# Performance work log

Hardware: AMD Instinct MI355X
Metric: run time of the kernel (lower is better)

The kernel has to match this reference:

```python
import jax, jax.numpy as jnp
import numpy as np

NUM_HEADS = 12


def setup_inputs() -> dict:
    key = jax.random.key(0)
    ks = jax.random.split(key, 6)
    dim = 384
    B, N = 2048, 49
    nW = 64
    return {
        "x": jax.random.normal(ks[0], (B, N, dim), dtype=jnp.float32),
        "mask": jax.random.normal(ks[1], (nW, N, N), dtype=jnp.float32),
        "qkv_w": jax.random.normal(ks[2], (3 * dim, dim), dtype=jnp.float32) * 0.02,
        "qkv_b": jax.random.normal(ks[3], (3 * dim,), dtype=jnp.float32) * 0.02,
        "proj_w": jax.random.normal(ks[4], (dim, dim), dtype=jnp.float32) * 0.02,
        "proj_b": jax.random.normal(ks[5], (dim,), dtype=jnp.float32) * 0.02,
    }


def reference(x, mask, qkv_w, qkv_b, proj_w, proj_b):
    B, N, C = x.shape
    H = NUM_HEADS
    Dh = C // H
    scale = Dh ** -0.5
    nW = mask.shape[0]

    # qkv projection: [B, N, 3C]
    qkv = x @ qkv_w.T + qkv_b
    q, k, v = jnp.split(qkv, 3, axis=-1)

    def heads(t):  # [B, N, C] -> [B, H, N, Dh]
        return t.reshape(B, N, H, Dh).transpose(0, 2, 1, 3)

    q, k, v = heads(q) * scale, heads(k), heads(v)

    # [B, H, N, N] attention scores
    attn = jnp.einsum("bhnd,bhmd->bhnm", q, k)
    # add per-window additive mask: reshape B -> (B//nW, nW)
    attn = attn.reshape(B // nW, nW, H, N, N) + mask[None, :, None, :, :]
    attn = jax.nn.softmax(attn.reshape(B, H, N, N), axis=-1)

    out = jnp.einsum("bhnm,bhmd->bhnd", attn, v)
    out = out.transpose(0, 2, 1, 3).reshape(B, N, C)
    return out @ proj_w.T + proj_b
```

## Files before the change

### kernel.cpp

```cpp
#include <hip/hip_runtime.h>
#include <hip/hip_bf16.h>
#include <stdint.h>

typedef unsigned short u16;
typedef __attribute__((ext_vector_type(8))) short short8;
typedef __attribute__((ext_vector_type(4))) float f32x4;

__device__ inline u16 f2bf(float f) {
    union { float f; unsigned int u; } x; x.f = f;
    unsigned int u = x.u;
    unsigned int r = (u + 0x7FFFu + ((u >> 16) & 1u)) >> 16;
    return (u16)r;
}

__device__ inline void gld_lds16(const u16* g, u16* l) {
    auto const* gp = reinterpret_cast<const __attribute__((address_space(1))) unsigned int*>(
        reinterpret_cast<uintptr_t>(g));
    auto* lp = reinterpret_cast<__attribute__((address_space(3))) unsigned int*>(
        reinterpret_cast<uintptr_t>(l));
    __builtin_amdgcn_global_load_lds(gp, lp, 16, 0, 0);
}

#define NX8 4816896
#define NQ8 55296
#define NP8 18432
__global__ __launch_bounds__(256) void prep_all(const float* __restrict__ x,
                                                const float* __restrict__ qw,
                                                const float* __restrict__ pw,
                                                u16* __restrict__ xb,
                                                u16* __restrict__ wq,
                                                u16* __restrict__ wp) {
    size_t i = (size_t)blockIdx.x * 256 + threadIdx.x;
    const float* src; u16* dst; size_t off;
    if (i < NX8)            { src = x;  dst = xb; off = i; }
    else if (i < NX8 + NQ8) { src = qw; dst = wq; off = i - NX8; }
    else                    { src = pw; dst = wp; off = i - (NX8 + NQ8); }
    float4 v0 = ((const float4*)src)[off * 2];
    float4 v1 = ((const float4*)src)[off * 2 + 1];
    u16 h[8];
    h[0] = f2bf(v0.x); h[1] = f2bf(v0.y); h[2] = f2bf(v0.z); h[3] = f2bf(v0.w);
    h[4] = f2bf(v1.x); h[5] = f2bf(v1.y); h[6] = f2bf(v1.z); h[7] = f2bf(v1.w);
    *(uint4*)(dst + off * 8) = *(const uint4*)h;
}

__global__ __launch_bounds__(256) void qkv_gemm(const u16* __restrict__ xb,
                                                const u16* __restrict__ wq,
                                                const float* __restrict__ bias,
                                                u16* __restrict__ qkv_out) {
    __shared__ u16 As[128 * 32];
    __shared__ u16 Bs[128 * 32];
    const int tid = threadIdx.x;
    const int wave = tid >> 6, lane = tid & 63;
    const int lr = lane >> 4, lc = lane & 15;
    const int wm = (wave & 1) * 64, wn = (wave >> 1) * 64;
    const int lin = blockIdx.x;
    const int xcd = lin & 7;
    const int idx = lin >> 3;
    const int nBase = (idx % 9) * 128;
    const int mBase = (xcd * 98 + idx / 9) * 128;

    f32x4 acc[4][4] = {};

    const int srow = lane >> 2, scol = (lane & 3) * 8;
    const u16* aSrc = xb + (size_t)(mBase + wave * 32 + srow) * 384 + scol;
    const u16* bSrc = wq + (size_t)(nBase + wave * 32 + srow) * 384 + scol;
    u16* aDst = &As[wave * 1024];
    u16* bDst = &Bs[wave * 1024];

    for (int k0 = 0; k0 < 384; k0 += 32) {
        gld_lds16(aSrc + k0, aDst);
        gld_lds16(aSrc + k0 + (size_t)16 * 384, aDst + 512);
        gld_lds16(bSrc + k0, bDst);
        gld_lds16(bSrc + k0 + (size_t)16 * 384, bDst + 512);
        __syncthreads();
        short8 af[4], bfr[4];
#pragma unroll
        for (int i = 0; i < 4; ++i)
            af[i] = *(const short8*)&As[(wm + i * 16 + lc) * 32 + lr * 8];
#pragma unroll
        for (int j = 0; j < 4; ++j)
            bfr[j] = *(const short8*)&Bs[(wn + j * 16 + lc) * 32 + lr * 8];
#pragma unroll
        for (int i = 0; i < 4; ++i)
#pragma unroll
            for (int j = 0; j < 4; ++j)
                acc[i][j] = __builtin_amdgcn_mfma_f32_16x16x32_bf16(af[i], bfr[j], acc[i][j], 0, 0, 0);
        __syncthreads();
    }

    const float scale = 0.17677669529663687f;
#pragma unroll
    for (int j = 0; j < 4; ++j) {
        int gn = nBase + wn + j * 16 + lc;
        int s = gn / 384;
        int rem = gn - s * 384;
        int h = rem >> 5, d = rem & 31;
        float bv = bias[gn];
        float mult = (s == 0) ? scale : 1.0f;
#pragma unroll
        for (int i = 0; i < 4; ++i) {
#pragma unroll
            for (int r = 0; r < 4; ++r) {
                int gm = mBase + wm + i * 16 + lr * 4 + r;
                int b = gm / 49;
                int tok = gm - b * 49;
                float val = (acc[i][j][r] + bv) * mult;
                qkv_out[(((size_t)(b * 12 + h) * 3 + s) * 49 + tok) * 32 + d] = f2bf(val);
            }
        }
    }
}

#define PST 68
__global__ __launch_bounds__(256, 3) void attn_kernel(const u16* __restrict__ qkv,
                                                      const float* __restrict__ mask,
                                                      u16* __restrict__ aout) {
    __shared__ u16 P_s[4][64 * PST];
    __shared__ u16 Vt_s[4][32 * PST];
    const int tid = threadIdx.x;
    const int wave = tid >> 6, lane = tid & 63;
    const int lr = lane >> 4, lc = lane & 15;
    const int bid = blockIdx.x;
    const int b = bid / 3;
    const int h = (bid - b * 3) * 4 + wave;
    const int w = b & 63;
    const float* mrow = mask + (size_t)w * 2401;

    const u16* base = qkv + (size_t)(b * 12 + h) * 3 * 49 * 32;
    const u16* Q = base;
    const u16* K = base + 49 * 32;
    const u16* V = base + 2 * 49 * 32;

    {
        u16 vv[32];
        if (lane < 49) {
#pragma unroll
            for (int c = 0; c < 4; ++c)
                *(uint4*)&vv[c * 8] = *(const uint4*)(V + lane * 32 + c * 8);
        } else {
#pragma unroll
            for (int c = 0; c < 32; ++c) vv[c] = 0;
        }
#pragma unroll
        for (int d = 0; d < 32; ++d)
            Vt_s[wave][d * PST + lane] = vv[d];
    }

    short8 qf[4], kf[4];
    const short8 z8 = {0, 0, 0, 0, 0, 0, 0, 0};
#pragma unroll
    for (int i = 0; i < 4; ++i) {
        int row = i * 16 + lc;
        qf[i] = (row < 49) ? *(const short8*)(Q + row * 32 + lr * 8) : z8;
        kf[i] = (row < 49) ? *(const short8*)(K + row * 32 + lr * 8) : z8;
    }
    __syncthreads();

    f32x4 S[4][4] = {};
#pragma unroll
    for (int i = 0; i < 4; ++i)
#pragma unroll
        for (int j = 0; j < 4; ++j)
            S[i][j] = __builtin_amdgcn_mfma_f32_16x16x32_bf16(qf[i], kf[j], S[i][j], 0, 0, 0);

    float l_sum[4][4];
#pragma unroll
    for (int si = 0; si < 4; ++si) {
#pragma unroll
        for (int r = 0; r < 4; ++r) {
            int i = si * 16 + lr * 4 + r;
            int im = (i < 49) ? i : 48;
            float s = 0.0f;
#pragma unroll
            for (int sj = 0; sj < 4; ++sj) {
                int jc = sj * 16 + lc;
                float t = (jc < 49) ? (S[si][sj][r] + mrow[im * 49 + jc]) : -1e30f;
                float p = __expf(t);
                s += p;
                S[si][sj][r] = p;
            }
            s += __shfl_xor(s, 1);
            s += __shfl_xor(s, 2);
            s += __shfl_xor(s, 4);
            s += __shfl_xor(s, 8);
            l_sum[si][r] = s;
        }
    }

#pragma unroll
    for (int si = 0; si < 4; ++si)
#pragma unroll
        for (int sj = 0; sj < 4; ++sj)
#pragma unroll
            for (int r = 0; r < 4; ++r) {
                int i = si * 16 + lr * 4 + r;
                int jc = sj * 16 + lc;
                P_s[wave][i * PST + jc] = f2bf(S[si][sj][r]);
            }
    __syncthreads();

    short8 vf[2][2];
#pragma unroll
    for (int nt = 0; nt < 2; ++nt)
#pragma unroll
        for (int kt = 0; kt < 2; ++kt)
            vf[nt][kt] = *(const short8*)&Vt_s[wave][(nt * 16 + lc) * PST + kt * 32 + lr * 8];

    f32x4 O[4][2] = {};
#pragma unroll
    for (int si = 0; si < 4; ++si) {
#pragma unroll
        for (int kt = 0; kt < 2; ++kt) {
            short8 pf = *(const short8*)&P_s[wave][(si * 16 + lc) * PST + kt * 32 + lr * 8];
#pragma unroll
            for (int nt = 0; nt < 2; ++nt)
                O[si][nt] = __builtin_amdgcn_mfma_f32_16x16x32_bf16(pf, vf[nt][kt], O[si][nt], 0, 0, 0);
        }
    }

#pragma unroll
    for (int si = 0; si < 4; ++si) {
#pragma unroll
        for (int nt = 0; nt < 2; ++nt) {
#pragma unroll
            for (int r = 0; r < 4; ++r) {
                int i = si * 16 + lr * 4 + r;
                if (i < 49) {
                    float val = O[si][nt][r] * __builtin_amdgcn_rcpf(l_sum[si][r]);
                    aout[(size_t)(b * 49 + i) * 384 + h * 32 + nt * 16 + lc] = f2bf(val);
                }
            }
        }
    }
}

__global__ __launch_bounds__(256) void proj_gemm(const u16* __restrict__ a,
                                                 const u16* __restrict__ wp,
                                                 const float* __restrict__ bias,
                                                 float* __restrict__ out) {
    __shared__ u16 As[128 * 32];
    __shared__ u16 Bs[128 * 32];
    const int tid = threadIdx.x;
    const int wave = tid >> 6, lane = tid & 63;
    const int lr = lane >> 4, lc = lane & 15;
    const int wm = (wave & 1) * 64, wn = (wave >> 1) * 64;
    const int lin = blockIdx.x;
    const int xcd = lin & 7;
    const int idx = lin >> 3;
    const int nBase = (idx % 3) * 128;
    const int mBase = (xcd * 98 + idx / 3) * 128;

    f32x4 acc[4][4] = {};

    const int srow = lane >> 2, scol = (lane & 3) * 8;
    const u16* aSrc = a  + (size_t)(mBase + wave * 32 + srow) * 384 + scol;
    const u16* bSrc = wp + (size_t)(nBase + wave * 32 + srow) * 384 + scol;
    u16* aDst = &As[wave * 1024];
    u16* bDst = &Bs[wave * 1024];

    for (int k0 = 0; k0 < 384; k0 += 32) {
        gld_lds16(aSrc + k0, aDst);
        gld_lds16(aSrc + k0 + (size_t)16 * 384, aDst + 512);
        gld_lds16(bSrc + k0, bDst);
        gld_lds16(bSrc + k0 + (size_t)16 * 384, bDst + 512);
        __syncthreads();
        short8 af[4], bfr[4];
#pragma unroll
        for (int i = 0; i < 4; ++i)
            af[i] = *(const short8*)&As[(wm + i * 16 + lc) * 32 + lr * 8];
#pragma unroll
        for (int j = 0; j < 4; ++j)
            bfr[j] = *(const short8*)&Bs[(wn + j * 16 + lc) * 32 + lr * 8];
#pragma unroll
        for (int i = 0; i < 4; ++i)
#pragma unroll
            for (int j = 0; j < 4; ++j)
                acc[i][j] = __builtin_amdgcn_mfma_f32_16x16x32_bf16(af[i], bfr[j], acc[i][j], 0, 0, 0);
        __syncthreads();
    }

#pragma unroll
    for (int j = 0; j < 4; ++j) {
        int gn = nBase + wn + j * 16 + lc;
        float bv = bias[gn];
#pragma unroll
        for (int i = 0; i < 4; ++i) {
#pragma unroll
            for (int r = 0; r < 4; ++r) {
                int gm = mBase + wm + i * 16 + lr * 4 + r;
                out[(size_t)gm * 384 + gn] = acc[i][j][r] + bv;
            }
        }
    }
}

extern "C" void kernel_launch(void* const* d_in, const int* in_sizes, int n_in,
                              void* d_out, int out_size, void* d_ws, size_t ws_size,
                              hipStream_t stream) {
    const float* x      = (const float*)d_in[0];
    const float* mask   = (const float*)d_in[1];
    const float* qkv_w  = (const float*)d_in[2];
    const float* qkv_b  = (const float*)d_in[3];
    const float* proj_w = (const float*)d_in[4];
    const float* proj_b = (const float*)d_in[5];
    float* out = (float*)d_out;

    char* ws = (char*)d_ws;
    u16* wq   = (u16*)ws;
    u16* wp   = (u16*)(ws + 884736);
    u16* qkvb = (u16*)(ws + 884736 + 294912);
    u16* xb   = (u16*)(ws + 884736 + 294912 + 231211008);
    u16* attn = xb;

    prep_all<<<19104, 256, 0, stream>>>(x, qkv_w, proj_w, xb, wq, wp);
    qkv_gemm<<<7056, 256, 0, stream>>>(xb, wq, qkv_b, qkvb);
    attn_kernel<<<6144, 256, 0, stream>>>(qkvb, mask, attn);
    proj_gemm<<<2352, 256, 0, stream>>>(attn, wp, proj_b, out);
}
```

Baseline: 606.1 us.

## Swap MFMA operands for vectorized epilogue stores and row-major QKV layout

Swaps the MFMA A/B operands in both GEMMs so each lane holds four consecutive output columns, which allows packed 8-byte bf16 stores and 16-byte float4 stores with vectorized bias loads. The QKV buffer changes from a per-head scattered layout to plain row-major [tokens, 1152], which removes the per-element div/mod index math. The attention kernel now reads Q/K/V with a 1152-element row stride, so its loads are more strided, which may cost some read efficiency.

```diff
diff --git a/kernel.cpp b/kernel.cpp
--- a/kernel.cpp
+++ b/kernel.cpp
@@ -84,29 +84,25 @@
         for (int i = 0; i < 4; ++i)
 #pragma unroll
             for (int j = 0; j < 4; ++j)
-                acc[i][j] = __builtin_amdgcn_mfma_f32_16x16x32_bf16(af[i], bfr[j], acc[i][j], 0, 0, 0);
+                acc[i][j] = __builtin_amdgcn_mfma_f32_16x16x32_bf16(bfr[j], af[i], acc[i][j], 0, 0, 0);
         __syncthreads();
     }
 
     const float scale = 0.17677669529663687f;
 #pragma unroll
     for (int j = 0; j < 4; ++j) {
-        int gn = nBase + wn + j * 16 + lc;
-        int s = gn / 384;
-        int rem = gn - s * 384;
-        int h = rem >> 5, d = rem & 31;
-        float bv = bias[gn];
-        float mult = (s == 0) ? scale : 1.0f;
+        int gnb = nBase + wn + j * 16 + lr * 4;
+        float4 bv = *(const float4*)&bias[gnb];
+        float mult = (gnb < 384) ? scale : 1.0f;
 #pragma unroll
         for (int i = 0; i < 4; ++i) {
-#pragma unroll
-            for (int r = 0; r < 4; ++r) {
-                int gm = mBase + wm + i * 16 + lr * 4 + r;
-                int b = gm / 49;
-                int tok = gm - b * 49;
-                float val = (acc[i][j][r] + bv) * mult;
-                qkv_out[(((size_t)(b * 12 + h) * 3 + s) * 49 + tok) * 32 + d] = f2bf(val);
-            }
+            int gm = mBase + wm + i * 16 + lc;
+            union { u16 h[4]; uint2 u; } pk;
+            pk.h[0] = f2bf((acc[i][j][0] + bv.x) * mult);
+            pk.h[1] = f2bf((acc[i][j][1] + bv.y) * mult);
+            pk.h[2] = f2bf((acc[i][j][2] + bv.z) * mult);
+            pk.h[3] = f2bf((acc[i][j][3] + bv.w) * mult);
+            *(uint2*)(qkv_out + (size_t)gm * 1152 + gnb) = pk.u;
         }
     }
 }
@@ -126,17 +122,16 @@
     const int w = b & 63;
     const float* mrow = mask + (size_t)w * 2401;
 
-    const u16* base = qkv + (size_t)(b * 12 + h) * 3 * 49 * 32;
-    const u16* Q = base;
-    const u16* K = base + 49 * 32;
-    const u16* V = base + 2 * 49 * 32;
+    const u16* Q = qkv + (size_t)b * 49 * 1152 + h * 32;
+    const u16* K = Q + 384;
+    const u16* V = Q + 768;
 
     {
         u16 vv[32];
         if (lane < 49) {
 #pragma unroll
             for (int c = 0; c < 4; ++c)
-                *(uint4*)&vv[c * 8] = *(const uint4*)(V + lane * 32 + c * 8);
+                *(uint4*)&vv[c * 8] = *(const uint4*)(V + (size_t)lane * 1152 + c * 8);
         } else {
 #pragma unroll
             for (int c = 0; c < 32; ++c) vv[c] = 0;
@@ -151,8 +146,8 @@
 #pragma unroll
     for (int i = 0; i < 4; ++i) {
         int row = i * 16 + lc;
-        qf[i] = (row < 49) ? *(const short8*)(Q + row * 32 + lr * 8) : z8;
-        kf[i] = (row < 49) ? *(const short8*)(K + row * 32 + lr * 8) : z8;
+        qf[i] = (row < 49) ? *(const short8*)(Q + (size_t)row * 1152 + lr * 8) : z8;
+        kf[i] = (row < 49) ? *(const short8*)(K + (size_t)row * 1152 + lr * 8) : z8;
     }
     __syncthreads();
 
@@ -275,21 +270,23 @@
         for (int i = 0; i < 4; ++i)
 #pragma unroll
             for (int j = 0; j < 4; ++j)
-                acc[i][j] = __builtin_amdgcn_mfma_f32_16x16x32_bf16(af[i], bfr[j], acc[i][j], 0, 0, 0);
+                acc[i][j] = __builtin_amdgcn_mfma_f32_16x16x32_bf16(bfr[j], af[i], acc[i][j], 0, 0, 0);
         __syncthreads();
     }
 
 #pragma unroll
     for (int j = 0; j < 4; ++j) {
-        int gn = nBase + wn + j * 16 + lc;
-        float bv = bias[gn];
+        int gnb = nBase + wn + j * 16 + lr * 4;
+        float4 bv = *(const float4*)&bias[gnb];
 #pragma unroll
         for (int i = 0; i < 4; ++i) {
-#pragma unroll
-            for (int r = 0; r < 4; ++r) {
-                int gm = mBase + wm + i * 16 + lr * 4 + r;
-                out[(size_t)gm * 384 + gn] = acc[i][j][r] + bv;
-            }
+            int gm = mBase + wm + i * 16 + lc;
+            float4 o;
+            o.x = acc[i][j][0] + bv.x;
+            o.y = acc[i][j][1] + bv.y;
+            o.z = acc[i][j][2] + bv.z;
+            o.w = acc[i][j][3] + bv.w;
+            *(float4*)(out + (size_t)gm * 384 + gnb) = o;
         }
     }
 }
```

After: 595.5 us. About the same (-1.7%).
